# Kernel optimization log

Hardware: AMD Instinct MI355X
Metric: run time of the kernel (lower is better)

The kernel has to match this reference:

```python
import jax, jax.numpy as jnp
import numpy as np

FS = 16000.0
Q = 2.0
MAX_MFC = 150.0
LP_CUTOFF = 2.5
ATT_FACTOR = 1.0  # dau1997 preset


def _mfc_array():
    # mfc = 0 (lowpass), 5, 10 Hz linear, then log-spaced with ratio r up to max_mfc
    mfc = [0.0, 5.0, 10.0]
    r = (1.0 + 1.0 / (2.0 * Q)) / (1.0 - 1.0 / (2.0 * Q))  # = 5/3 for Q=2
    f = 10.0 * r
    while f <= MAX_MFC:
        mfc.append(f)
        f *= r
    return np.array(mfc, dtype=np.float64)  # 8 entries for the defaults


def _butter2_lp(fcut, fs):
    # 2nd-order Butterworth lowpass via bilinear transform (matches scipy.signal.butter)
    K = np.tan(np.pi * fcut / fs)
    n = 1.0 / (1.0 + np.sqrt(2.0) * K + K * K)
    b = np.array([K * K, 2.0 * K * K, K * K]) * n
    a = np.array([1.0, 2.0 * (K * K - 1.0) * n, (1.0 - np.sqrt(2.0) * K + K * K) * n])
    return b, a


def setup_inputs() -> dict:
    key = jax.random.key(0)
    x = jax.random.normal(key, (4, 31, 48000), dtype=jnp.float32)  # [B, F, T]
    return {"x": x}


def reference(x):
    B, F, T = x.shape
    N = B * F
    xr = x.reshape(N, T)

    # ---- mfc = 0 filter: 2nd-order Butterworth lowpass @ 2.5 Hz, DF2T scan ----
    b_np, a_np = _butter2_lp(LP_CUTOFF, FS)
    b = jnp.asarray(b_np, jnp.float32)
    a = jnp.asarray(a_np, jnp.float32)

    def lp_step(state, xt):  # state [N,2], xt [N]
        y = b[0] * xt + state[:, 0]
        s0 = b[1] * xt - a[1] * y + state[:, 1]
        s1 = b[2] * xt - a[2] * y
        return jnp.stack([s0, s1], axis=1), y

    _, ylp = jax.lax.scan(lp_step, jnp.zeros((N, 2), jnp.float32), xr.T)
    ylp = 2.0 * ylp.T  # [N, T], factor 2 = 6 dB emphasis

    # ---- bandpass efilt: complex first-order resonators ----
    mfc = _mfc_array()[1:]                      # [M] bandpass center freqs
    bw = np.where(mfc <= 10.0, 5.0, mfc / Q)    # 5 Hz bandwidth for linear part
    e0 = np.exp(-np.pi * bw / FS)               # exp(-(2*pi*bw/fs)/2)
    b0 = jnp.asarray((1.0 - e0).astype(np.complex64))
    cpole = jnp.asarray((e0 * np.exp(1j * 2.0 * np.pi * mfc / FS)).astype(np.complex64))
    M = mfc.shape[0]

    def bp_step(yprev, xt):  # yprev [N,M] complex, xt [N] complex
        y = b0[None, :] * xt[:, None] + cpole[None, :] * yprev
        return y, y

    _, ybp = jax.lax.scan(bp_step, jnp.zeros((N, M), jnp.complex64),
                          xr.T.astype(jnp.complex64))
    ybp = 2.0 * jnp.moveaxis(ybp, 0, -1)        # [N, M, T]

    # phase preserved for mfc <= 10 Hz (real part), envelope (abs) above
    keep_phase = jnp.asarray(mfc <= 10.0)
    out_bp = jnp.where(keep_phase[None, :, None], jnp.real(ybp), ATT_FACTOR * jnp.abs(ybp))

    out = jnp.concatenate([ylp[:, None, :], out_bp], axis=1)  # [N, 1+M, T]
    return out.reshape(B, F, 1 + M, T)
```

## Files before the change

kernel.cpp:

```cpp
#include <hip/hip_runtime.h>
#include <cmath>

#define T_LEN 48000
#define L_CHUNK 128
#define N_CHUNKS 375
#define N_ROWS 124
#define SLOTS 1024
#define ROWS_PER_BLK 64
#define XS_STRIDE 132
#define TR_STRIDE 20
#define GRP 15
#define NGRP 25

struct CoefF {
    float lp_b0, lp_b1, lp_b2, lp_a1, lp_a2;
    float bp_b0[7], bp_cr[7], bp_ci[7];
};
struct CoefD {
    double p00, p01, p10, p11;
    double Pr[7], Pi[7];
};

__device__ __forceinline__ void sel_M(int ch, const CoefD& D,
                                      double& m00, double& m01, double& m10, double& m11) {
    if (ch == 0) {
        m00 = D.p00; m01 = D.p01; m10 = D.p10; m11 = D.p11;
    } else {
        double Pr = 0.0, Pi = 0.0;
#pragma unroll
        for (int c = 1; c < 8; ++c) if (ch == c) { Pr = D.Pr[c - 1]; Pi = D.Pi[c - 1]; }
        m00 = Pr; m01 = -Pi; m10 = Pi; m11 = Pr;
    }
}

template <bool FINAL>
__global__ __launch_bounds__(512) void mfb_chunk(const float* __restrict__ x,
                                                 CoefF C,
                                                 float2* __restrict__ ws_fin,
                                                 const float2* __restrict__ ws_init,
                                                 float* __restrict__ out) {
    extern __shared__ __align__(16) float smem[];
    float* xs = smem;
    const int t     = threadIdx.x;
    const int j     = blockIdx.y;
    const int n0    = (int)blockIdx.x * ROWS_PER_BLK;
    const int tbase = j * L_CHUNK;

#pragma unroll
    for (int i = 0; i < 4; ++i) {
        int g = i * 512 + t;
        int r = g >> 5, c = (g & 31) * 4;
        int n = n0 + r;
        float4 v = make_float4(0.f, 0.f, 0.f, 0.f);
        if (n < N_ROWS)
            v = *reinterpret_cast<const float4*>(x + (size_t)n * T_LEN + tbase + c);
        *reinterpret_cast<float4*>(xs + r * XS_STRIDE + c) = v;
    }
    __syncthreads();

    const int ch   = t >> 6;
    const int nn   = t & 63;
    const int n    = n0 + nn;
    const int widx = j * SLOTS + ch * 128 + n;
    float* trw = smem + ROWS_PER_BLK * XS_STRIDE + ch * (64 * TR_STRIDE);

    float f_b0, f_b1 = 0.f, f_b2 = 0.f, f_a1 = 0.f, f_a2 = 0.f, f_cr = 0.f, f_ci = 0.f;
    if (ch == 0) {
        f_b0 = C.lp_b0; f_b1 = C.lp_b1; f_b2 = C.lp_b2; f_a1 = C.lp_a1; f_a2 = C.lp_a2;
    } else {
        f_b0 = 0.f;
#pragma unroll
        for (int c = 1; c < 8; ++c)
            if (ch == c) { f_b0 = C.bp_b0[c - 1]; f_cr = C.bp_cr[c - 1]; f_ci = C.bp_ci[c - 1]; }
    }
    const bool kp = (ch <= 2);

    float s0 = 0.f, s1 = 0.f;
    if (FINAL) { float2 u = ws_init[widx]; s0 = u.x; s1 = u.y; }

    for (int b = 0; b < L_CHUNK / 16; ++b) {
        float4 xv4[4];
#pragma unroll
        for (int q = 0; q < 4; ++q)
            xv4[q] = *reinterpret_cast<const float4*>(xs + nn * XS_STRIDE + b * 16 + q * 4);
        const float* xv = reinterpret_cast<const float*>(xv4);

        float buf[16];
        if (ch == 0) {
#pragma unroll
            for (int k = 0; k < 16; ++k) {
                float xvk = xv[k];
                float y  = fmaf(f_b0, xvk, s0);
                s0 = fmaf(f_b1, xvk, fmaf(-f_a1, y, s1));
                s1 = fmaf(f_b2, xvk, -f_a2 * y);
                if (FINAL) buf[k] = 2.0f * y;
            }
        } else {
#pragma unroll
            for (int k = 0; k < 16; ++k) {
                float xvk = xv[k];
                float nyr = fmaf(f_cr, s0, fmaf(-f_ci, s1, f_b0 * xvk));
                float nyi = fmaf(f_cr, s1, f_ci * s0);
                s0 = nyr; s1 = nyi;
                if (FINAL)
                    buf[k] = kp ? 2.0f * nyr : 2.0f * sqrtf(fmaf(nyr, nyr, nyi * nyi));
            }
        }

        if (FINAL) {
            asm volatile("s_waitcnt lgkmcnt(0)" ::: "memory");
            *reinterpret_cast<float4*>(trw + nn * TR_STRIDE + 0)  = make_float4(buf[0], buf[1], buf[2], buf[3]);
            *reinterpret_cast<float4*>(trw + nn * TR_STRIDE + 4)  = make_float4(buf[4], buf[5], buf[6], buf[7]);
            *reinterpret_cast<float4*>(trw + nn * TR_STRIDE + 8)  = make_float4(buf[8], buf[9], buf[10], buf[11]);
            *reinterpret_cast<float4*>(trw + nn * TR_STRIDE + 12) = make_float4(buf[12], buf[13], buf[14], buf[15]);
            asm volatile("s_waitcnt lgkmcnt(0)" ::: "memory");
#pragma unroll
            for (int s = 0; s < 4; ++s) {
                int rr = s * 16 + (nn >> 2);
                int kk = (nn & 3) * 4;
                int nrow = n0 + rr;
                if (nrow < N_ROWS) {
                    float4 v = *reinterpret_cast<const float4*>(trw + rr * TR_STRIDE + kk);
                    *reinterpret_cast<float4*>(out + (size_t)(nrow * 8 + ch) * T_LEN
                                               + tbase + b * 16 + kk) = v;
                }
            }
        }
    }
    if (!FINAL) ws_fin[widx] = make_float2(s0, s1);
}

__global__ __launch_bounds__(256) void mfb_groupsum(const float2* __restrict__ ws_fin,
                                                    float2* __restrict__ A, CoefD D) {
    int tid = blockIdx.x * 256 + (int)threadIdx.x;
    int s = tid & 1023, g = tid >> 10;
    double m00, m01, m10, m11;
    sel_M(s >> 7, D, m00, m01, m10, m11);

    const float2* base = ws_fin + (size_t)g * GRP * SLOTS + s;
    float2 f[GRP];
#pragma unroll
    for (int i = 0; i < GRP; ++i) f[i] = base[(size_t)i * SLOTS];

    double a0 = 0.0, a1 = 0.0;
#pragma unroll
    for (int i = 0; i < GRP; ++i) {
        double t0 = m00 * a0 + m01 * a1 + (double)f[i].x;
        double t1 = m10 * a0 + m11 * a1 + (double)f[i].y;
        a0 = t0; a1 = t1;
    }
    A[(size_t)g * SLOTS + s] = make_float2((float)a0, (float)a1);
}

__global__ __launch_bounds__(256) void mfb_groupscan(const float2* __restrict__ A,
                                                     float2* __restrict__ U, CoefD D15) {
    int s = blockIdx.x * 256 + (int)threadIdx.x;
    double m00, m01, m10, m11;
    sel_M(s >> 7, D15, m00, m01, m10, m11);

    float2 f[NGRP];
#pragma unroll
    for (int g = 0; g < NGRP; ++g) f[g] = A[(size_t)g * SLOTS + s];

    double u0 = 0.0, u1 = 0.0;
#pragma unroll
    for (int g = 0; g < NGRP; ++g) {
        U[(size_t)g * SLOTS + s] = make_float2((float)u0, (float)u1);
        double t0 = (double)f[g].x + m00 * u0 + m01 * u1;
        double t1 = (double)f[g].y + m10 * u0 + m11 * u1;
        u0 = t0; u1 = t1;
    }
}

__global__ __launch_bounds__(256) void mfb_expand(const float2* __restrict__ ws_fin,
                                                  const float2* __restrict__ U,
                                                  float2* __restrict__ ws_init, CoefD D) {
    int tid = blockIdx.x * 256 + (int)threadIdx.x;
    int s = tid & 1023, g = tid >> 10;
    double m00, m01, m10, m11;
    sel_M(s >> 7, D, m00, m01, m10, m11);

    const float2* base = ws_fin + (size_t)g * GRP * SLOTS + s;
    float2 f[GRP];
#pragma unroll
    for (int i = 0; i < GRP; ++i) f[i] = base[(size_t)i * SLOTS];

    float2 ug = U[(size_t)g * SLOTS + s];
    double u0 = ug.x, u1 = ug.y;
#pragma unroll
    for (int i = 0; i < GRP; ++i) {
        ws_init[(size_t)(g * GRP + i) * SLOTS + s] = make_float2((float)u0, (float)u1);
        double t0 = (double)f[i].x + m00 * u0 + m01 * u1;
        double t1 = (double)f[i].y + m10 * u0 + m11 * u1;
        u0 = t0; u1 = t1;
    }
}

extern "C" void kernel_launch(void* const* d_in, const int* in_sizes, int n_in,
                              void* d_out, int out_size, void* d_ws, size_t ws_size,
                              hipStream_t stream) {
    const float* x = (const float*)d_in[0];
    float* out = (float*)d_out;
    char* ws = (char*)d_ws;
    float2* ws_fin  = (float2*)ws;
    float2* ws_init = (float2*)(ws + 3072000);
    float2* Agg     = (float2*)(ws + 6144000);
    float2* Upre    = (float2*)(ws + 6348800);

    const double PI = 3.141592653589793;
    const double FS = 16000.0;
    CoefF C; CoefD D, D15;
    {
        double K   = tan(PI * 2.5 / FS);
        double nrm = 1.0 / (1.0 + sqrt(2.0) * K + K * K);
        double a1  = 2.0 * (K * K - 1.0) * nrm;
        double a2  = (1.0 - sqrt(2.0) * K + K * K) * nrm;
        C.lp_b0 = (float)(K * K * nrm);
        C.lp_b1 = (float)(2.0 * K * K * nrm);
        C.lp_b2 = (float)(K * K * nrm);
        C.lp_a1 = (float)a1;
        C.lp_a2 = (float)a2;
        double p00 = -a1, p01 = 1.0, p10 = -a2, p11 = 0.0;
        for (int i = 0; i < 7; ++i) {
            double q00 = p00 * p00 + p01 * p10, q01 = p00 * p01 + p01 * p11;
            double q10 = p10 * p00 + p11 * p10, q11 = p10 * p01 + p11 * p11;
            p00 = q00; p01 = q01; p10 = q10; p11 = q11;
        }
        D.p00 = p00; D.p01 = p01; D.p10 = p10; D.p11 = p11;
        double r00 = 1, r01 = 0, r10 = 0, r11 = 1, b00 = p00, b01 = p01, b10 = p10, b11 = p11;
        for (int e = 15; e > 0; e >>= 1) {
            if (e & 1) {
                double q00 = r00 * b00 + r01 * b10, q01 = r00 * b01 + r01 * b11;
                double q10 = r10 * b00 + r11 * b10, q11 = r10 * b01 + r11 * b11;
                r00 = q00; r01 = q01; r10 = q10; r11 = q11;
            }
            double q00 = b00 * b00 + b01 * b10, q01 = b00 * b01 + b01 * b11;
            double q10 = b10 * b00 + b11 * b10, q11 = b10 * b01 + b11 * b11;
            b00 = q00; b01 = q01; b10 = q10; b11 = q11;
        }
        D15.p00 = r00; D15.p01 = r01; D15.p10 = r10; D15.p11 = r11;

        double rr = (1.0 + 1.0 / 4.0) / (1.0 - 1.0 / 4.0);
        double mfc[7]; mfc[0] = 5.0; mfc[1] = 10.0;
        double f = 10.0 * rr;
        for (int m = 2; m < 7; ++m) { mfc[m] = f; f *= rr; }
        for (int m = 0; m < 7; ++m) {
            double bw = (mfc[m] <= 10.0) ? 5.0 : mfc[m] * 0.5;
            double e0 = exp(-PI * bw / FS);
            double th = 2.0 * PI * mfc[m] / FS;
            C.bp_b0[m] = (float)(1.0 - e0);
            C.bp_cr[m] = (float)(e0 * cos(th));
            C.bp_ci[m] = (float)(e0 * sin(th));
            double eL  = exp(-PI * bw * (double)L_CHUNK / FS);
            double ang = th * (double)L_CHUNK;
            D.Pr[m] = eL * cos(ang);
            D.Pi[m] = eL * sin(ang);
            double eG  = exp(-PI * bw * (double)(L_CHUNK * GRP) / FS);
            double angG = th * (double)(L_CHUNK * GRP);
            D15.Pr[m] = eG * cos(angG);
            D15.Pi[m] = eG * sin(angG);
        }
    }

    const int smem1 = ROWS_PER_BLK * XS_STRIDE * 4;
    const int smem3 = smem1 + 8 * 64 * TR_STRIDE * 4;
    dim3 grid(2, N_CHUNKS);
    mfb_chunk<false><<<grid, 512, smem1, stream>>>(x, C, ws_fin, nullptr, nullptr);
    mfb_groupsum<<<100, 256, 0, stream>>>(ws_fin, Agg, D);
    mfb_groupscan<<<4, 256, 0, stream>>>(Agg, Upre, D15);
    mfb_expand<<<100, 256, 0, stream>>>(ws_fin, Upre, ws_init, D);
    mfb_chunk<true><<<grid, 512, smem3, stream>>>(x, C, nullptr, ws_init, out);
}
```

Baseline: 70.79 us.

## Fuse carry expansion into final chunk kernel and drop explicit LDS waitcnts

Removes the separate expand kernel. Each thread in the final chunk pass now reconstructs its own initial filter state from the group prefix and the preceding chunk finals inside the group, computed in double precision. This eliminates one kernel launch and the write/read of the per-chunk init-state buffer, at the cost of redundant serial double-precision recurrence steps (up to 14) per thread. It also replaces the hard s_waitcnt asm around the LDS transpose with compiler-only barriers, relying on the compiler to insert the required waits.

```diff
diff --git a/kernel.cpp b/kernel.cpp
--- a/kernel.cpp
+++ b/kernel.cpp
@@ -35,9 +35,9 @@
 
 template <bool FINAL>
 __global__ __launch_bounds__(512) void mfb_chunk(const float* __restrict__ x,
-                                                 CoefF C,
+                                                 CoefF C, CoefD D,
                                                  float2* __restrict__ ws_fin,
-                                                 const float2* __restrict__ ws_init,
+                                                 const float2* __restrict__ U,
                                                  float* __restrict__ out) {
     extern __shared__ __align__(16) float smem[];
     float* xs = smem;
@@ -61,7 +61,7 @@
     const int ch   = t >> 6;
     const int nn   = t & 63;
     const int n    = n0 + nn;
-    const int widx = j * SLOTS + ch * 128 + n;
+    const int slot = ch * 128 + n;
     float* trw = smem + ROWS_PER_BLK * XS_STRIDE + ch * (64 * TR_STRIDE);
 
     float f_b0, f_b1 = 0.f, f_b2 = 0.f, f_a1 = 0.f, f_a2 = 0.f, f_cr = 0.f, f_ci = 0.f;
@@ -76,7 +76,26 @@
     const bool kp = (ch <= 2);
 
     float s0 = 0.f, s1 = 0.f;
-    if (FINAL) { float2 u = ws_init[widx]; s0 = u.x; s1 = u.y; }
+    if (FINAL) {
+        const int g = j / GRP, i = j - g * GRP;
+        double m00, m01, m10, m11;
+        sel_M(ch, D, m00, m01, m10, m11);
+        float2 ug = U[(size_t)g * SLOTS + slot];
+        double u0 = ug.x, u1 = ug.y;
+        const float2* Fb = ws_fin + (size_t)(g * GRP) * SLOTS + slot;
+        float2 f[GRP - 1];
+#pragma unroll
+        for (int k = 0; k < GRP - 1; ++k)
+            f[k] = (k < i) ? Fb[(size_t)k * SLOTS] : make_float2(0.f, 0.f);
+#pragma unroll
+        for (int k = 0; k < GRP - 1; ++k)
+            if (k < i) {
+                double t0 = (double)f[k].x + m00 * u0 + m01 * u1;
+                double t1 = (double)f[k].y + m10 * u0 + m11 * u1;
+                u0 = t0; u1 = t1;
+            }
+        s0 = (float)u0; s1 = (float)u1;
+    }
 
     for (int b = 0; b < L_CHUNK / 16; ++b) {
         float4 xv4[4];
@@ -108,12 +127,12 @@
         }
 
         if (FINAL) {
-            asm volatile("s_waitcnt lgkmcnt(0)" ::: "memory");
+            asm volatile("" ::: "memory");
             *reinterpret_cast<float4*>(trw + nn * TR_STRIDE + 0)  = make_float4(buf[0], buf[1], buf[2], buf[3]);
             *reinterpret_cast<float4*>(trw + nn * TR_STRIDE + 4)  = make_float4(buf[4], buf[5], buf[6], buf[7]);
             *reinterpret_cast<float4*>(trw + nn * TR_STRIDE + 8)  = make_float4(buf[8], buf[9], buf[10], buf[11]);
             *reinterpret_cast<float4*>(trw + nn * TR_STRIDE + 12) = make_float4(buf[12], buf[13], buf[14], buf[15]);
-            asm volatile("s_waitcnt lgkmcnt(0)" ::: "memory");
+            asm volatile("" ::: "memory");
 #pragma unroll
             for (int s = 0; s < 4; ++s) {
                 int rr = s * 16 + (nn >> 2);
@@ -127,7 +146,7 @@
             }
         }
     }
-    if (!FINAL) ws_fin[widx] = make_float2(s0, s1);
+    if (!FINAL) ws_fin[(size_t)j * SLOTS + slot] = make_float2(s0, s1);
 }
 
 __global__ __launch_bounds__(256) void mfb_groupsum(const float2* __restrict__ ws_fin,
@@ -168,30 +187,6 @@
         U[(size_t)g * SLOTS + s] = make_float2((float)u0, (float)u1);
         double t0 = (double)f[g].x + m00 * u0 + m01 * u1;
         double t1 = (double)f[g].y + m10 * u0 + m11 * u1;
-        u0 = t0; u1 = t1;
-    }
-}
-
-__global__ __launch_bounds__(256) void mfb_expand(const float2* __restrict__ ws_fin,
-                                                  const float2* __restrict__ U,
-                                                  float2* __restrict__ ws_init, CoefD D) {
-    int tid = blockIdx.x * 256 + (int)threadIdx.x;
-    int s = tid & 1023, g = tid >> 10;
-    double m00, m01, m10, m11;
-    sel_M(s >> 7, D, m00, m01, m10, m11);
-
-    const float2* base = ws_fin + (size_t)g * GRP * SLOTS + s;
-    float2 f[GRP];
-#pragma unroll
-    for (int i = 0; i < GRP; ++i) f[i] = base[(size_t)i * SLOTS];
-
-    float2 ug = U[(size_t)g * SLOTS + s];
-    double u0 = ug.x, u1 = ug.y;
-#pragma unroll
-    for (int i = 0; i < GRP; ++i) {
-        ws_init[(size_t)(g * GRP + i) * SLOTS + s] = make_float2((float)u0, (float)u1);
-        double t0 = (double)f[i].x + m00 * u0 + m01 * u1;
-        double t1 = (double)f[i].y + m10 * u0 + m11 * u1;
         u0 = t0; u1 = t1;
     }
 }
@@ -203,9 +198,8 @@
     float* out = (float*)d_out;
     char* ws = (char*)d_ws;
     float2* ws_fin  = (float2*)ws;
-    float2* ws_init = (float2*)(ws + 3072000);
-    float2* Agg     = (float2*)(ws + 6144000);
-    float2* Upre    = (float2*)(ws + 6348800);
+    float2* Agg     = (float2*)(ws + 3072000);
+    float2* Upre    = (float2*)(ws + 3276800);
 
     const double PI = 3.141592653589793;
     const double FS = 16000.0;
@@ -265,9 +259,8 @@
     const int smem1 = ROWS_PER_BLK * XS_STRIDE * 4;
     const int smem3 = smem1 + 8 * 64 * TR_STRIDE * 4;
     dim3 grid(2, N_CHUNKS);
-    mfb_chunk<false><<<grid, 512, smem1, stream>>>(x, C, ws_fin, nullptr, nullptr);
+    mfb_chunk<false><<<grid, 512, smem1, stream>>>(x, C, D, ws_fin, nullptr, nullptr);
     mfb_groupsum<<<100, 256, 0, stream>>>(ws_fin, Agg, D);
     mfb_groupscan<<<4, 256, 0, stream>>>(Agg, Upre, D15);
-    mfb_expand<<<100, 256, 0, stream>>>(ws_fin, Upre, ws_init, D);
-    mfb_chunk<true><<<grid, 512, smem3, stream>>>(x, C, nullptr, ws_init, out);
-}
+    mfb_chunk<true><<<grid, 512, smem3, stream>>>(x, C, D, ws_fin, Upre, out);
+}
```

Result: no change. 69.96 us (median of 3 runs) (-1.2%).
